# Performance work log

Measured on AMD Instinct MI355X. Metric: run time of the kernel, lower is better.

Reference implementation:

```python
import jax, jax.numpy as jnp
import numpy as np

N0, N1, N2 = 400000, 40000, 4000   # source nodes, layer-1 targets, layer-2 targets
E1, E2 = 640000, 64000             # sampled edges per bipartite block (avg deg 16)
IN, HID, OUT = 128, 256, 64


def setup_inputs() -> dict:
    key = jax.random.key(0)
    ks = jax.random.split(key, 11)
    x = jax.random.normal(ks[0], (N0, IN), jnp.float32)
    src1 = jax.random.randint(ks[1], (E1,), 0, N0)
    dst1 = jax.random.randint(ks[2], (E1,), 0, N1)
    src2 = jax.random.randint(ks[3], (E2,), 0, N1)
    dst2 = jax.random.randint(ks[4], (E2,), 0, N2)
    # SAGEConv params (PyG default: mean aggr, lin_l on aggregated msgs w/ bias, lin_r on root)
    s_in, s_hid = 1.0 / np.sqrt(IN), 1.0 / np.sqrt(HID)
    w_l1 = jax.random.uniform(ks[5], (IN, HID), jnp.float32, -s_in, s_in)
    b_l1 = jnp.zeros((HID,), jnp.float32)
    w_r1 = jax.random.uniform(ks[6], (IN, HID), jnp.float32, -s_in, s_in)
    w_l2 = jax.random.uniform(ks[7], (HID, OUT), jnp.float32, -s_hid, s_hid)
    b_l2 = jnp.zeros((OUT,), jnp.float32)
    w_r2 = jax.random.uniform(ks[8], (HID, OUT), jnp.float32, -s_hid, s_hid)
    return dict(x=x, src1=src1, dst1=dst1, src2=src2, dst2=dst2,
                w_l1=w_l1, b_l1=b_l1, w_r1=w_r1,
                w_l2=w_l2, b_l2=b_l2, w_r2=w_r2,
                n1=N1, n2=N2)


def _sage_conv(x_src, x_tgt, src, dst, w_l, b_l, w_r, n_tgt):
    # mean aggregation of neighbor features onto targets
    msg = x_src[src]                                             # [E, F] gather
    agg = jax.ops.segment_sum(msg, dst, num_segments=n_tgt)      # [n_tgt, F] scatter-add
    deg = jax.ops.segment_sum(jnp.ones_like(dst, x_src.dtype), dst, num_segments=n_tgt)
    agg = agg / jnp.maximum(deg, 1.0)[:, None]
    return agg @ w_l + b_l + x_tgt @ w_r


def reference(x, src1, dst1, src2, dst2, w_l1, b_l1, w_r1, w_l2, b_l2, w_r2, n1, n2):
    # layer 1: bipartite block (N0 sources -> n1 targets), targets are prefix of sources
    h = _sage_conv(x, x[:n1], src1, dst1, w_l1, b_l1, w_r1, n1)
    h = jax.nn.relu(h)  # eval mode: dropout is identity
    # layer 2: (n1 sources -> n2 targets)
    out = _sage_conv(h, h[:n2], src2, dst2, w_l2, b_l2, w_r2, n2)
    return jax.nn.log_softmax(out, axis=-1)
```

## Files before the change

kernel.cpp:

```cpp
#include <hip/hip_runtime.h>
#include <math.h>

#define IN   128
#define HID  256
#define OUT  64
#define N0   400000
#define N1T  40000
#define N2T  4000
#define E1   640000
#define E2   64000

__global__ __launch_bounds__(256) void hist_kernel(
    const int* __restrict__ dst1, const int* __restrict__ dst2,
    int* __restrict__ cnt1, int* __restrict__ cnt2)
{
    int e = blockIdx.x * 256 + threadIdx.x;
    if (e < E1) {
        atomicAdd(&cnt1[dst1[e]], 1);
    } else if (e < E1 + E2) {
        atomicAdd(&cnt2[dst2[e - E1]], 1);
    }
}

__global__ __launch_bounds__(1024) void scan_kernel(
    const int* __restrict__ cnt, int* __restrict__ off, int* __restrict__ cur, int n)
{
    __shared__ int sums[1024];
    const int t = threadIdx.x;
    const int chunk = (n + 1023) >> 10;
    const int begin = t * chunk;
    const int end = min(begin + chunk, n);

    int s = 0;
    for (int i = begin; i < end; ++i) s += cnt[i];
    sums[t] = s;
    __syncthreads();

    for (int d = 1; d < 1024; d <<= 1) {
        int tmp = (t >= d) ? sums[t - d] : 0;
        __syncthreads();
        sums[t] += tmp;
        __syncthreads();
    }

    int run = sums[t] - s;
    for (int i = begin; i < end; ++i) {
        off[i] = run;
        cur[i] = run;
        run += cnt[i];
    }
    if (end == n && begin < n) off[n] = run;
    if (n == 0 && t == 0) off[0] = 0;
}

__global__ __launch_bounds__(256) void scatter_idx_kernel(
    const int* __restrict__ src1, const int* __restrict__ dst1,
    const int* __restrict__ src2, const int* __restrict__ dst2,
    int* __restrict__ cur1, int* __restrict__ cur2,
    int* __restrict__ ss1, int* __restrict__ ss2)
{
    int e = blockIdx.x * 256 + threadIdx.x;
    if (e < E1) {
        int pos = atomicAdd(&cur1[dst1[e]], 1);
        ss1[pos] = src1[e];
    } else if (e < E1 + E2) {
        int ee = e - E1;
        int pos = atomicAdd(&cur2[dst2[ee]], 1);
        ss2[pos] = src2[ee];
    }
}

__global__ __launch_bounds__(256) void gather1_kernel(
    const float* __restrict__ x,
    const int* __restrict__ off, const int* __restrict__ ss,
    float* __restrict__ agg)
{
    int row = blockIdx.x * 4 + (threadIdx.x >> 6);
    if (row >= N1T) return;
    int lane = threadIdx.x & 63;
    int b = off[row], en = off[row + 1];

    float2 acc = make_float2(0.0f, 0.0f);
    for (int e = b; e < en; ++e) {
        int s = ss[e];
        float2 v = reinterpret_cast<const float2*>(x + (size_t)s * IN)[lane];
        acc.x += v.x;
        acc.y += v.y;
    }
    float inv = 1.0f / fmaxf((float)(en - b), 1.0f);
    acc.x *= inv;
    acc.y *= inv;
    reinterpret_cast<float2*>(agg + (size_t)row * IN)[lane] = acc;
}

__global__ __launch_bounds__(256) void gather2_kernel(
    const float* __restrict__ h,
    const int* __restrict__ off, const int* __restrict__ ss,
    float* __restrict__ agg)
{
    int row = blockIdx.x * 4 + (threadIdx.x >> 6);
    if (row >= N2T) return;
    int lane = threadIdx.x & 63;
    int b = off[row], en = off[row + 1];

    float4 acc = make_float4(0.0f, 0.0f, 0.0f, 0.0f);
    for (int e = b; e < en; ++e) {
        int s = ss[e];
        float4 v = reinterpret_cast<const float4*>(h + (size_t)s * HID)[lane];
        acc.x += v.x; acc.y += v.y; acc.z += v.z; acc.w += v.w;
    }
    float inv = 1.0f / fmaxf((float)(en - b), 1.0f);
    acc.x *= inv; acc.y *= inv; acc.z *= inv; acc.w *= inv;
    reinterpret_cast<float4*>(agg + (size_t)row * HID)[lane] = acc;
}

__global__ __launch_bounds__(256) void layer1_kernel(
    const float* __restrict__ x,
    const float* __restrict__ agg,
    const float* __restrict__ w_l, const float* __restrict__ b_l,
    const float* __restrict__ w_r, float* __restrict__ h)
{
    __shared__ float a_s[16][IN];
    __shared__ float x_s[16][IN];
    const int r0 = blockIdx.x * 16;
    const int tid = threadIdx.x;

    for (int i = tid; i < 16 * IN; i += 256) {
        int r = i >> 7;
        int k = i & 127;
        a_s[r][k] = agg[(size_t)(r0 + r) * IN + k];
        x_s[r][k] = x[(size_t)(r0 + r) * IN + k];
    }
    __syncthreads();

    float acc[16];
#pragma unroll
    for (int r = 0; r < 16; ++r) acc[r] = 0.0f;

    const int j = tid;
    for (int k = 0; k < IN; ++k) {
        float wl = w_l[k * HID + j];
        float wr = w_r[k * HID + j];
#pragma unroll
        for (int r = 0; r < 16; ++r)
            acc[r] += a_s[r][k] * wl + x_s[r][k] * wr;
    }

    float b = b_l[j];
#pragma unroll
    for (int r = 0; r < 16; ++r) {
        h[(size_t)(r0 + r) * HID + j] = fmaxf(acc[r] + b, 0.0f);
    }
}

__global__ __launch_bounds__(64) void layer2_kernel(
    const float* __restrict__ h,
    const float* __restrict__ agg,
    const float* __restrict__ w_l, const float* __restrict__ b_l,
    const float* __restrict__ w_r, float* __restrict__ out)
{
    __shared__ float a_s[HID];
    __shared__ float h_s[HID];
    const int i = blockIdx.x;
    const int j = threadIdx.x;

    const float4* ar = reinterpret_cast<const float4*>(agg + (size_t)i * HID);
    const float4* hr = reinterpret_cast<const float4*>(h + (size_t)i * HID);
    reinterpret_cast<float4*>(a_s)[j] = ar[j];
    reinterpret_cast<float4*>(h_s)[j] = hr[j];
    __syncthreads();

    float acc = b_l[j];
    for (int k = 0; k < HID; ++k) {
        acc += a_s[k] * w_l[k * OUT + j] + h_s[k] * w_r[k * OUT + j];
    }

    float m = acc;
#pragma unroll
    for (int off = 32; off; off >>= 1) m = fmaxf(m, __shfl_xor(m, off));
    float ex = expf(acc - m);
#pragma unroll
    for (int off = 32; off; off >>= 1) ex += __shfl_xor(ex, off);
    out[(size_t)i * OUT + j] = acc - m - logf(ex);
}

extern "C" void kernel_launch(void* const* d_in, const int* in_sizes, int n_in,
                              void* d_out, int out_size, void* d_ws, size_t ws_size,
                              hipStream_t stream)
{
    const float* x    = (const float*)d_in[0];
    const int*   src1 = (const int*)  d_in[1];
    const int*   dst1 = (const int*)  d_in[2];
    const int*   src2 = (const int*)  d_in[3];
    const int*   dst2 = (const int*)  d_in[4];
    const float* w_l1 = (const float*)d_in[5];
    const float* b_l1 = (const float*)d_in[6];
    const float* w_r1 = (const float*)d_in[7];
    const float* w_l2 = (const float*)d_in[8];
    const float* b_l2 = (const float*)d_in[9];
    const float* w_r2 = (const float*)d_in[10];
    float* out = (float*)d_out;

    int* ws_i = (int*)d_ws;
    int* cnt1 = ws_i;
    int* cnt2 = cnt1 + N1T;
    int* off1 = cnt2 + N2T;
    int* off2 = off1 + N1T + 1;
    int* cur1 = off2 + N2T + 1;
    int* cur2 = cur1 + N1T;
    int* ss1  = cur2 + N2T;
    int* ss2  = ss1 + E1;
    float* agg1 = (float*)(ss2 + E2);
    float* agg2 = agg1 + (size_t)N1T * IN;
    float* h    = agg2 + (size_t)N2T * HID;

    hipMemsetAsync(cnt1, 0, (N1T + N2T) * sizeof(int), stream);

    const int ET = E1 + E2;
    hist_kernel<<<(ET + 255) / 256, 256, 0, stream>>>(dst1, dst2, cnt1, cnt2);
    scan_kernel<<<1, 1024, 0, stream>>>(cnt1, off1, cur1, N1T);
    scan_kernel<<<1, 1024, 0, stream>>>(cnt2, off2, cur2, N2T);
    scatter_idx_kernel<<<(ET + 255) / 256, 256, 0, stream>>>(src1, dst1, src2, dst2,
                                                             cur1, cur2, ss1, ss2);
    gather1_kernel<<<(N1T + 3) / 4, 256, 0, stream>>>(x, off1, ss1, agg1);
    layer1_kernel<<<N1T / 16, 256, 0, stream>>>(x, agg1, w_l1, b_l1, w_r1, h);
    gather2_kernel<<<(N2T + 3) / 4, 256, 0, stream>>>(h, off2, ss2, agg2);
    layer2_kernel<<<N2T, 64, 0, stream>>>(h, agg2, w_l2, b_l2, w_r2, out);
}
```

Baseline: 734.7 us.

## Register-tile layer1 GEMM, batch neighbor index loads, merge scan launches

Layer1 now stages 64 rows of agg and x transposed in shared memory and gives each thread a 16x4 register tile with float4 weight loads, so each weight load is reused across more rows. The gather kernels load up to 64 neighbor indices with one coalesced read, broadcast them with shuffles and unroll the row loads so more memory requests are in flight. The two scan launches are merged into one two-block launch. The larger register tile raises register pressure and may lower occupancy, and the 64KB shared buffer limits how many blocks fit per CU.

```diff
diff --git a/kernel.cpp b/kernel.cpp
--- a/kernel.cpp
+++ b/kernel.cpp
@@ -22,13 +22,18 @@
     }
 }
 
-__global__ __launch_bounds__(1024) void scan_kernel(
-    const int* __restrict__ cnt, int* __restrict__ off, int* __restrict__ cur, int n)
-{
+__global__ __launch_bounds__(1024) void scan2_kernel(
+    const int* __restrict__ cnt1, int* __restrict__ off1, int* __restrict__ cur1,
+    const int* __restrict__ cnt2, int* __restrict__ off2, int* __restrict__ cur2)
+{
+    const int* cnt; int* off; int* cur; int n;
+    if (blockIdx.x == 0) { cnt = cnt1; off = off1; cur = cur1; n = N1T; }
+    else                 { cnt = cnt2; off = off2; cur = cur2; n = N2T; }
+
     __shared__ int sums[1024];
     const int t = threadIdx.x;
     const int chunk = (n + 1023) >> 10;
-    const int begin = t * chunk;
+    const int begin = min(t * chunk, n);
     const int end = min(begin + chunk, n);
 
     int s = 0;
@@ -49,8 +54,7 @@
         cur[i] = run;
         run += cnt[i];
     }
-    if (end == n && begin < n) off[n] = run;
-    if (n == 0 && t == 0) off[0] = 0;
+    if (end == n && begin < end) off[n] = run;
 }
 
 __global__ __launch_bounds__(256) void scatter_idx_kernel(
@@ -81,11 +85,28 @@
     int b = off[row], en = off[row + 1];
 
     float2 acc = make_float2(0.0f, 0.0f);
-    for (int e = b; e < en; ++e) {
-        int s = ss[e];
-        float2 v = reinterpret_cast<const float2*>(x + (size_t)s * IN)[lane];
-        acc.x += v.x;
-        acc.y += v.y;
+    for (int base = b; base < en; base += 64) {
+        int cnt = min(64, en - base);
+        int myidx = (lane < cnt) ? ss[base + lane] : 0;
+        int e = 0;
+        for (; e + 4 <= cnt; e += 4) {
+            int s0 = __shfl(myidx, e);
+            int s1 = __shfl(myidx, e + 1);
+            int s2 = __shfl(myidx, e + 2);
+            int s3 = __shfl(myidx, e + 3);
+            float2 v0 = reinterpret_cast<const float2*>(x + (size_t)s0 * IN)[lane];
+            float2 v1 = reinterpret_cast<const float2*>(x + (size_t)s1 * IN)[lane];
+            float2 v2 = reinterpret_cast<const float2*>(x + (size_t)s2 * IN)[lane];
+            float2 v3 = reinterpret_cast<const float2*>(x + (size_t)s3 * IN)[lane];
+            acc.x += v0.x + v1.x + v2.x + v3.x;
+            acc.y += v0.y + v1.y + v2.y + v3.y;
+        }
+        for (; e < cnt; ++e) {
+            int s = __shfl(myidx, e);
+            float2 v = reinterpret_cast<const float2*>(x + (size_t)s * IN)[lane];
+            acc.x += v.x;
+            acc.y += v.y;
+        }
     }
     float inv = 1.0f / fmaxf((float)(en - b), 1.0f);
     acc.x *= inv;
@@ -104,10 +125,23 @@
     int b = off[row], en = off[row + 1];
 
     float4 acc = make_float4(0.0f, 0.0f, 0.0f, 0.0f);
-    for (int e = b; e < en; ++e) {
-        int s = ss[e];
-        float4 v = reinterpret_cast<const float4*>(h + (size_t)s * HID)[lane];
-        acc.x += v.x; acc.y += v.y; acc.z += v.z; acc.w += v.w;
+    for (int base = b; base < en; base += 64) {
+        int cnt = min(64, en - base);
+        int myidx = (lane < cnt) ? ss[base + lane] : 0;
+        int e = 0;
+        for (; e + 2 <= cnt; e += 2) {
+            int s0 = __shfl(myidx, e);
+            int s1 = __shfl(myidx, e + 1);
+            float4 v0 = reinterpret_cast<const float4*>(h + (size_t)s0 * HID)[lane];
+            float4 v1 = reinterpret_cast<const float4*>(h + (size_t)s1 * HID)[lane];
+            acc.x += v0.x + v1.x; acc.y += v0.y + v1.y;
+            acc.z += v0.z + v1.z; acc.w += v0.w + v1.w;
+        }
+        for (; e < cnt; ++e) {
+            int s = __shfl(myidx, e);
+            float4 v = reinterpret_cast<const float4*>(h + (size_t)s * HID)[lane];
+            acc.x += v.x; acc.y += v.y; acc.z += v.z; acc.w += v.w;
+        }
     }
     float inv = 1.0f / fmaxf((float)(en - b), 1.0f);
     acc.x *= inv; acc.y *= inv; acc.z *= inv; acc.w *= inv;
@@ -120,36 +154,75 @@
     const float* __restrict__ w_l, const float* __restrict__ b_l,
     const float* __restrict__ w_r, float* __restrict__ h)
 {
-    __shared__ float a_s[16][IN];
-    __shared__ float x_s[16][IN];
-    const int r0 = blockIdx.x * 16;
+    __shared__ float A_s[256][64];
+    const int r0 = blockIdx.x * 64;
     const int tid = threadIdx.x;
 
-    for (int i = tid; i < 16 * IN; i += 256) {
-        int r = i >> 7;
-        int k = i & 127;
-        a_s[r][k] = agg[(size_t)(r0 + r) * IN + k];
-        x_s[r][k] = x[(size_t)(r0 + r) * IN + k];
+    for (int i = tid; i < 64 * 32; i += 256) {
+        int r = i >> 5;
+        int c4 = i & 31;
+        float4 va = reinterpret_cast<const float4*>(agg + (size_t)(r0 + r) * IN)[c4];
+        float4 vx = reinterpret_cast<const float4*>(x + (size_t)(r0 + r) * IN)[c4];
+        int k = c4 * 4;
+        A_s[k + 0][r] = va.x; A_s[k + 1][r] = va.y;
+        A_s[k + 2][r] = va.z; A_s[k + 3][r] = va.w;
+        A_s[128 + k + 0][r] = vx.x; A_s[128 + k + 1][r] = vx.y;
+        A_s[128 + k + 2][r] = vx.z; A_s[128 + k + 3][r] = vx.w;
     }
     __syncthreads();
 
-    float acc[16];
-#pragma unroll
-    for (int r = 0; r < 16; ++r) acc[r] = 0.0f;
-
-    const int j = tid;
-    for (int k = 0; k < IN; ++k) {
-        float wl = w_l[k * HID + j];
-        float wr = w_r[k * HID + j];
-#pragma unroll
-        for (int r = 0; r < 16; ++r)
-            acc[r] += a_s[r][k] * wl + x_s[r][k] * wr;
-    }
-
-    float b = b_l[j];
-#pragma unroll
-    for (int r = 0; r < 16; ++r) {
-        h[(size_t)(r0 + r) * HID + j] = fmaxf(acc[r] + b, 0.0f);
+    const int ngrp = tid & 63;
+    const int mgrp = tid >> 6;
+
+    float acc[16][4];
+#pragma unroll
+    for (int m = 0; m < 16; ++m)
+#pragma unroll
+        for (int j = 0; j < 4; ++j) acc[m][j] = 0.0f;
+
+    const float4* wl4 = reinterpret_cast<const float4*>(w_l);
+    const float4* wr4 = reinterpret_cast<const float4*>(w_r);
+
+#pragma unroll 4
+    for (int k = 0; k < 128; ++k) {
+        float4 w = wl4[k * 64 + ngrp];
+        const float4* ap = reinterpret_cast<const float4*>(&A_s[k][mgrp * 16]);
+        float4 a0 = ap[0], a1 = ap[1], a2 = ap[2], a3 = ap[3];
+        float am[16] = {a0.x, a0.y, a0.z, a0.w, a1.x, a1.y, a1.z, a1.w,
+                        a2.x, a2.y, a2.z, a2.w, a3.x, a3.y, a3.z, a3.w};
+#pragma unroll
+        for (int m = 0; m < 16; ++m) {
+            acc[m][0] += am[m] * w.x;
+            acc[m][1] += am[m] * w.y;
+            acc[m][2] += am[m] * w.z;
+            acc[m][3] += am[m] * w.w;
+        }
+    }
+#pragma unroll 4
+    for (int k = 0; k < 128; ++k) {
+        float4 w = wr4[k * 64 + ngrp];
+        const float4* ap = reinterpret_cast<const float4*>(&A_s[128 + k][mgrp * 16]);
+        float4 a0 = ap[0], a1 = ap[1], a2 = ap[2], a3 = ap[3];
+        float am[16] = {a0.x, a0.y, a0.z, a0.w, a1.x, a1.y, a1.z, a1.w,
+                        a2.x, a2.y, a2.z, a2.w, a3.x, a3.y, a3.z, a3.w};
+#pragma unroll
+        for (int m = 0; m < 16; ++m) {
+            acc[m][0] += am[m] * w.x;
+            acc[m][1] += am[m] * w.y;
+            acc[m][2] += am[m] * w.z;
+            acc[m][3] += am[m] * w.w;
+        }
+    }
+
+    float4 b = reinterpret_cast<const float4*>(b_l)[ngrp];
+#pragma unroll
+    for (int m = 0; m < 16; ++m) {
+        float4 o;
+        o.x = fmaxf(acc[m][0] + b.x, 0.0f);
+        o.y = fmaxf(acc[m][1] + b.y, 0.0f);
+        o.z = fmaxf(acc[m][2] + b.z, 0.0f);
+        o.w = fmaxf(acc[m][3] + b.w, 0.0f);
+        reinterpret_cast<float4*>(h + (size_t)(r0 + mgrp * 16 + m) * HID)[ngrp] = o;
     }
 }
 
@@ -218,12 +291,11 @@
 
     const int ET = E1 + E2;
     hist_kernel<<<(ET + 255) / 256, 256, 0, stream>>>(dst1, dst2, cnt1, cnt2);
-    scan_kernel<<<1, 1024, 0, stream>>>(cnt1, off1, cur1, N1T);
-    scan_kernel<<<1, 1024, 0, stream>>>(cnt2, off2, cur2, N2T);
+    scan2_kernel<<<2, 1024, 0, stream>>>(cnt1, off1, cur1, cnt2, off2, cur2);
     scatter_idx_kernel<<<(ET + 255) / 256, 256, 0, stream>>>(src1, dst1, src2, dst2,
                                                              cur1, cur2, ss1, ss2);
     gather1_kernel<<<(N1T + 3) / 4, 256, 0, stream>>>(x, off1, ss1, agg1);
-    layer1_kernel<<<N1T / 16, 256, 0, stream>>>(x, agg1, w_l1, b_l1, w_r1, h);
+    layer1_kernel<<<N1T / 64, 256, 0, stream>>>(x, agg1, w_l1, b_l1, w_r1, h);
     gather2_kernel<<<(N2T + 3) / 4, 256, 0, stream>>>(h, off2, ss2, agg2);
     layer2_kernel<<<N2T, 64, 0, stream>>>(h, agg2, w_l2, b_l2, w_r2, out);
 }
```

After: 604.8 us. -17.7%, faster.
